# Kernel optimization log

Measured on AMD Instinct MI355X. Metric: run time of the kernel, lower is better.

Reference implementation:

```python
import jax, jax.numpy as jnp
import numpy as np


def _spectral_normalize(W):
    # spectral_norm divides the weight by its largest singular value
    sigma = jnp.linalg.norm(W, ord=2)
    return W / sigma


def setup_inputs() -> dict:
    key = jax.random.key(0)
    ks = jax.random.split(key, 8)
    B, C, H, W = 2, 64, 96, 96
    C8 = C // 8
    x = jax.random.normal(ks[0], (B, C, H, W), dtype=jnp.float32)
    Wq = jax.random.normal(ks[1], (C8, C), dtype=jnp.float32) * 0.1
    bq = jax.random.normal(ks[2], (C8,), dtype=jnp.float32) * 0.1
    Wk = jax.random.normal(ks[3], (C8, C), dtype=jnp.float32) * 0.1
    bk = jax.random.normal(ks[4], (C8,), dtype=jnp.float32) * 0.1
    Wv = jax.random.normal(ks[5], (C, C), dtype=jnp.float32) * 0.1
    bv = jax.random.normal(ks[6], (C,), dtype=jnp.float32) * 0.1
    gamma = jnp.ones((1,), dtype=jnp.float32)
    return {"x": x, "Wq": Wq, "bq": bq, "Wk": Wk, "bk": bk,
            "Wv": Wv, "bv": bv, "gamma": gamma}


def reference(x, Wq, bq, Wk, bk, Wv, bv, gamma):
    B, C, H, W = x.shape
    xf = x.reshape(B, C, H * W)                       # [B, C, N]
    Wq_n = _spectral_normalize(Wq)
    Wk_n = _spectral_normalize(Wk)
    Wv_n = _spectral_normalize(Wv)
    # 1x1 Conv1d == matmul over channel dim
    f = jnp.einsum('oc,bcn->bon', Wq_n, xf) + bq[None, :, None]   # [B, C/8, N]
    g = jnp.einsum('oc,bcn->bon', Wk_n, xf) + bk[None, :, None]   # [B, C/8, N]
    h = jnp.einsum('oc,bcn->bon', Wv_n, xf) + bv[None, :, None]   # [B, C, N]
    # scores[b,i,j] = sum_c f[b,c,i] * g[b,c,j];  softmax over dim=1 (i)
    scores = jnp.einsum('bci,bcj->bij', f, g)                      # [B, N, N]
    beta = jax.nn.softmax(scores, axis=1)
    # o[b,c,j] = sum_i h[b,c,i] * beta[b,i,j]
    o = gamma[0] * jnp.einsum('bci,bij->bcj', h, beta) + xf
    return o.reshape(B, C, H, W)
```

## Files before the change

### kernel.cpp

```cpp
#include <hip/hip_runtime.h>


#define N_PIX 9216
#define N_B   2
#define N_C   64

typedef _Float16 half8  __attribute__((ext_vector_type(8)));
typedef _Float16 half2v __attribute__((ext_vector_type(2)));
typedef float    float4v __attribute__((ext_vector_type(4)));
typedef float    float16v __attribute__((ext_vector_type(16)));
typedef int      int4v  __attribute__((ext_vector_type(4)));

#define LOG2E 1.44269504088896340736f
#define EXP_SHIFT 12.0f

__global__ __launch_bounds__(64) void k_sigma(const float* __restrict__ Wq,
                                              const float* __restrict__ Wk,
                                              const float* __restrict__ Wv,
                                              float* __restrict__ sig,
                                              unsigned* __restrict__ maxKu) {
  __shared__ float G8[8][8];
  __shared__ float Wl[64 * 64];
  __shared__ _Float16 Wh[64 * 80];
  __shared__ _Float16 Gh[64 * 80];
  const int t = threadIdx.x;
  const int mat = blockIdx.x;
  if (mat == 0 && t < 2) maxKu[t] = 0u;
  if (mat < 2) {
    const float* W = (mat == 0) ? Wq : Wk;
    const int i = t >> 3, j = t & 7;
    float g = 0.f;
    for (int c = 0; c < 64; ++c) g += W[i * 64 + c] * W[j * 64 + c];
    G8[i][j] = g;
    __syncthreads();
    const int L = t & 7;
    float G0[8], Gr[8];
    for (int k = 0; k < 8; ++k) { G0[k] = G8[L][k]; Gr[k] = G0[k]; }
    for (int it = 0; it < 8; ++it) {
      float g2[8] = {0, 0, 0, 0, 0, 0, 0, 0};
      for (int k = 0; k < 8; ++k) {
        float gik = Gr[k];
        for (int jj = 0; jj < 8; ++jj) g2[jj] += gik * __shfl(Gr[jj], k, 64);
      }
      float mx = 0.f;
      for (int jj = 0; jj < 8; ++jj) mx = fmaxf(mx, fabsf(g2[jj]));
      for (int d = 1; d < 8; d <<= 1) mx = fmaxf(mx, __shfl_xor(mx, d, 64));
      float r = 1.f / mx;
      for (int jj = 0; jj < 8; ++jj) Gr[jj] = g2[jj] * r;
    }
    float u = 0.f;
    for (int jj = 0; jj < 8; ++jj) u += Gr[jj];
    float y = 0.f;
    for (int k = 0; k < 8; ++k) y += G0[k] * __shfl(u, k, 64);
    float nu = u * y, de = u * u;
    for (int d = 1; d < 8; d <<= 1) { nu += __shfl_xor(nu, d, 64); de += __shfl_xor(de, d, 64); }
    if (t == 0) sig[mat] = sqrtf(nu / de);
  } else {
    for (int idx = t; idx < 4096; idx += 64) Wl[idx] = Wv[idx];
    __syncthreads();
    for (int idx = t; idx < 4096; idx += 64) Wh[(idx >> 6) * 80 + (idx & 63)] = (_Float16)Wl[idx];
    __syncthreads();
    const int lane15 = t & 15, quad = t >> 4;
    half8 fr[4][2];
    for (int rb = 0; rb < 4; ++rb)
      for (int kc = 0; kc < 2; ++kc)
        fr[rb][kc] = *(const half8*)&Wh[(lane15 + 16 * rb) * 80 + 32 * kc + 8 * quad];
    float4v D[4][4];
    for (int mb = 0; mb < 4; ++mb) for (int nb = 0; nb < 4; ++nb) D[mb][nb] = (float4v){0.f, 0.f, 0.f, 0.f};
    for (int kc = 0; kc < 2; ++kc)
      for (int mb = 0; mb < 4; ++mb)
        for (int nb = 0; nb < 4; ++nb)
          D[mb][nb] = __builtin_amdgcn_mfma_f32_16x16x32_f16(fr[mb][kc], fr[nb][kc], D[mb][nb], 0, 0, 0);
    for (int it = 0; it < 8; ++it) {
      float mx = 0.f;
      for (int mb = 0; mb < 4; ++mb) for (int nb = 0; nb < 4; ++nb) for (int r = 0; r < 4; ++r)
        mx = fmaxf(mx, fabsf(D[mb][nb][r]));
      for (int d = 1; d < 64; d <<= 1) mx = fmaxf(mx, __shfl_xor(mx, d, 64));
      float rs = 1.f / mx;
      for (int mb = 0; mb < 4; ++mb) for (int nb = 0; nb < 4; ++nb) for (int r = 0; r < 4; ++r)
        Gh[(4 * quad + r + 16 * mb) * 80 + lane15 + 16 * nb] = (_Float16)(D[mb][nb][r] * rs);
      __syncthreads();
      if (it == 7) break;
      for (int rb = 0; rb < 4; ++rb)
        for (int kc = 0; kc < 2; ++kc)
          fr[rb][kc] = *(const half8*)&Gh[(lane15 + 16 * rb) * 80 + 32 * kc + 8 * quad];
      for (int mb = 0; mb < 4; ++mb) for (int nb = 0; nb < 4; ++nb) D[mb][nb] = (float4v){0.f, 0.f, 0.f, 0.f};
      for (int kc = 0; kc < 2; ++kc)
        for (int mb = 0; mb < 4; ++mb)
          for (int nb = 0; nb < 4; ++nb)
            D[mb][nb] = __builtin_amdgcn_mfma_f32_16x16x32_f16(fr[mb][kc], fr[nb][kc], D[mb][nb], 0, 0, 0);
      __syncthreads();
    }
    float u = 0.f;
    for (int c = 0; c < 64; ++c) u += (float)Gh[t * 80 + c];
    float z = 0.f;
    for (int i2 = 0; i2 < 64; ++i2) z += Wl[i2 * 64 + t] * __shfl(u, i2, 64);
    float nu = z * z, de = u * u;
    for (int d = 1; d < 64; d <<= 1) { nu += __shfl_xor(nu, d, 64); de += __shfl_xor(de, d, 64); }
    if (t == 0) sig[2] = sqrtf(nu / de);
  }
}

__global__ __launch_bounds__(256) void k_fgh(const float* __restrict__ x,
                                             const float* __restrict__ Wq, const float* __restrict__ bq,
                                             const float* __restrict__ Wk, const float* __restrict__ bk,
                                             const float* __restrict__ Wv, const float* __restrict__ bv,
                                             const float* __restrict__ sig,
                                             _Float16* __restrict__ K16,
                                             _Float16* __restrict__ Q16,
                                             _Float16* __restrict__ VT16,
                                             unsigned* __restrict__ maxKu) {
  __shared__ _Float16 Wsh[80 * 64];
  __shared__ float bsh[80];
  const int t = threadIdx.x;
  const float iq = LOG2E / sig[0], ik = 1.0f / sig[1], iv = 1.0f / sig[2];
  for (int idx = t; idx < 80 * 64; idx += 256) {
    const int m = idx >> 6, c = idx & 63;
    float v;
    if (m < 8)       v = Wq[m * 64 + c] * iq;
    else if (m < 16) v = Wk[(m - 8) * 64 + c] * ik;
    else             v = Wv[(m - 16) * 64 + c] * iv;
    Wsh[idx] = (_Float16)v;
  }
  if (t < 80) {
    float v;
    if (t < 8)       v = bq[t] * LOG2E;
    else if (t < 16) v = bk[t - 8];
    else             v = bv[t - 16];
    bsh[t] = v;
  }
  __syncthreads();
  const int wave = t >> 6;
  const int lane = t & 63;
  const int lane15 = lane & 15, quad = lane >> 4;
  const int tile = blockIdx.x * 4 + wave;
  const int b = tile / 576;
  const int n = (tile % 576) * 16 + lane15;
  half8 wf[5][2];
  for (int mb = 0; mb < 5; ++mb)
    for (int kc = 0; kc < 2; ++kc)
      wf[mb][kc] = *(const half8*)&Wsh[(lane15 + 16 * mb) * 64 + 32 * kc + 8 * quad];
  float4v acc[5];
  for (int mb = 0; mb < 5; ++mb) acc[mb] = *(const float4v*)&bsh[16 * mb + 4 * quad];
  const float* xb = x + (size_t)b * N_C * N_PIX;
  for (int kc = 0; kc < 2; ++kc) {
    half8 bf;
    for (int j = 0; j < 8; ++j)
      bf[j] = (_Float16)xb[(size_t)(32 * kc + 8 * quad + j) * N_PIX + n];
    for (int mb = 0; mb < 5; ++mb)
      acc[mb] = __builtin_amdgcn_mfma_f32_16x16x32_f16(wf[mb][kc], bf, acc[mb], 0, 0, 0);
  }
  {
    _Float16* dstK = K16 + ((size_t)b * N_PIX + n) * 8;
    _Float16* dstQ = Q16 + ((size_t)b * N_PIX + n) * 8;
    for (int r = 0; r < 4; ++r) {
      const int m = 4 * quad + r;
      const _Float16 v = (_Float16)acc[0][r];
      if (m < 8) dstK[m] = v; else dstQ[m - 8] = v;
    }
  }
  for (int mb = 1; mb < 5; ++mb)
    for (int r = 0; r < 4; ++r) {
      const int c = 4 * quad + r + 16 * (mb - 1);
      VT16[((size_t)b * N_C + c) * N_PIX + n] = (_Float16)acc[mb][r];
    }
  float sq = 0.f;
  if (quad < 2)
    for (int r = 0; r < 4; ++r) sq += acc[0][r] * acc[0][r];
  sq += __shfl_xor(sq, 16, 64);
  for (int d = 1; d < 64; d <<= 1) sq = fmaxf(sq, __shfl_xor(sq, d, 64));
  if (lane == 0) atomicMax(&maxKu[b], __float_as_uint(sq));
}


__device__ __forceinline__ void gload16(const _Float16* g, _Float16* l) {
  __builtin_amdgcn_global_load_lds(
      (const __attribute__((address_space(1))) void*)g,
      (__attribute__((address_space(3))) void*)l, 16, 0, 0);
}
#define VMWAIT5() asm volatile("s_waitcnt vmcnt(5)" ::: "memory")

__global__ __launch_bounds__(256, 3) void k_attn(const _Float16* __restrict__ K16,
                                                 const _Float16* __restrict__ Q16,
                                                 const _Float16* __restrict__ VT16,
                                                 const unsigned* __restrict__ maxKu,
                                                 const float* __restrict__ x,
                                                 const float* __restrict__ gamma,
                                                 float* __restrict__ out) {
  __shared__ __align__(16) _Float16 SM[4][5120];
  const int wave = threadIdx.x >> 6;
  const int lane = threadIdx.x & 63;
  const int q31 = lane & 31, hi = lane >> 5;
  const int tile = blockIdx.x;
  const int b = tile / 288;
  const int jb = (tile % 288) * 32;
  const float gm = gamma[0];
  const _Float16* Kb = K16 + (size_t)b * N_PIX * 8;
  const _Float16* Vb = VT16 + (size_t)b * N_C * N_PIX;
  _Float16* Rg = SM[wave];
  const int cl = lane >> 2, kk = lane & 3;
  const int gsw = (kk ^ (cl & 3)) * 8;
  const int vq = q31 * 32;
  const int voff00 = vq + (((0 + hi) ^ (q31 & 3)) << 3);
  const int voff01 = vq + (((2 + hi) ^ (q31 & 3)) << 3);
  const int voff10 = 1024 + voff00;
  const int voff11 = 1024 + voff01;

  half8 qf = {};
  if (hi == 0) qf = *(const half8*)(Q16 + ((size_t)b * N_PIX + jb + q31) * 8);
  const float maxK = sqrtf(__uint_as_float(maxKu[b]));
  float nq = 0.f;
#pragma unroll
  for (int j = 0; j < 8; ++j) nq += (float)qf[j] * (float)qf[j];
  nq += __shfl_xor(nq, 32, 64);
  const float M = sqrtf(nq) * maxK - EXP_SHIFT;
  float16v sinit;
#pragma unroll
  for (int r2 = 0; r2 < 16; ++r2) sinit[r2] = -M;

  float16v acc0 = {}, acc1 = {};
  float ls = 0.f;

#define STAGE(SLOT, I0)                                                          \
  {                                                                              \
    const int _i = (I0);                                                         \
    gload16(Kb + (size_t)(_i + q31) * 8, Rg + 4096 + (SLOT) * 512);              \
    gload16(Vb + (size_t)cl * N_PIX + _i + gsw,        Rg + (SLOT) * 2048);      \
    gload16(Vb + (size_t)(16 + cl) * N_PIX + _i + gsw, Rg + (SLOT) * 2048 + 512);\
    gload16(Vb + (size_t)(32 + cl) * N_PIX + _i + gsw, Rg + (SLOT) * 2048 + 1024);\
    gload16(Vb + (size_t)(48 + cl) * N_PIX + _i + gsw, Rg + (SLOT) * 2048 + 1536);\
  }

  STAGE(0, 32 * wave)

#pragma unroll 1
  for (int r = 0; r < 72; ++r) {
    const int slot = r & 1, nslot = slot ^ 1;
    const int i1 = (r < 71) ? (128 * (r + 1) + 32 * wave) : (128 * 71 + 32 * wave);
    STAGE(nslot, i1)
    VMWAIT5();
    half8 kf = *(const half8*)&Rg[4096 + slot * 512 + q31 * 8];
    if (hi) kf = (half8){};
    float16v s = __builtin_amdgcn_mfma_f32_32x32x16_f16(kf, qf, sinit, 0, 0, 0);
    int pk[8];
#pragma unroll
    for (int u = 0; u < 8; ++u) {
      const float p0 = __builtin_amdgcn_exp2f(s[2 * u]);
      const float p1 = __builtin_amdgcn_exp2f(s[2 * u + 1]);
      ls += p0 + p1;
      pk[u] = __builtin_bit_cast(int, __builtin_amdgcn_cvt_pkrtz(p0, p1));
    }
    const int t0 = hi ? pk[0] : pk[2];
    const int t1 = hi ? pk[1] : pk[3];
    const int t2 = hi ? pk[4] : pk[6];
    const int t3 = hi ? pk[5] : pk[7];
    const int x0 = __shfl_xor(t0, 32, 64);
    const int x1 = __shfl_xor(t1, 32, 64);
    const int x2 = __shfl_xor(t2, 32, 64);
    const int x3 = __shfl_xor(t3, 32, 64);
    int4v B0i, B1i;
    B0i[0] = hi ? x0 : pk[0];  B0i[1] = hi ? x1 : pk[1];
    B0i[2] = hi ? pk[2] : x0;  B0i[3] = hi ? pk[3] : x1;
    B1i[0] = hi ? x2 : pk[4];  B1i[1] = hi ? x3 : pk[5];
    B1i[2] = hi ? pk[6] : x2;  B1i[3] = hi ? pk[7] : x3;
    const half8 P0 = __builtin_bit_cast(half8, B0i);
    const half8 P1 = __builtin_bit_cast(half8, B1i);
    const _Float16* Vs = Rg + slot * 2048;
    const half8 v00 = *(const half8*)&Vs[voff00];
    const half8 v01 = *(const half8*)&Vs[voff01];
    const half8 v10 = *(const half8*)&Vs[voff10];
    const half8 v11 = *(const half8*)&Vs[voff11];
    acc0 = __builtin_amdgcn_mfma_f32_32x32x16_f16(v00, P0, acc0, 0, 0, 0);
    acc0 = __builtin_amdgcn_mfma_f32_32x32x16_f16(v01, P1, acc0, 0, 0, 0);
    acc1 = __builtin_amdgcn_mfma_f32_32x32x16_f16(v10, P0, acc1, 0, 0, 0);
    acc1 = __builtin_amdgcn_mfma_f32_32x32x16_f16(v11, P1, acc1, 0, 0, 0);
  }
#undef STAGE
  asm volatile("s_waitcnt vmcnt(0)" ::: "memory");

  float* Ow = (float*)Rg;
  float* Lw = (float*)Rg + 1100;
  ls += __shfl_xor(ls, 32, 64);
  if (hi == 0) Lw[q31] = ls;
#pragma unroll
  for (int r2 = 0; r2 < 16; ++r2) Ow[lane * 17 + r2] = acc0[r2];
  __syncthreads();
  float ltot = 0.f;
#pragma unroll
  for (int w = 0; w < 4; ++w) ltot += ((const float*)SM[w])[1100 + q31];
  const float inv = gm / ltot;
  const float* xb = x + (size_t)b * N_C * N_PIX;
  float* ob = out + (size_t)b * N_C * N_PIX;
#pragma unroll
  for (int r2 = 0; r2 < 16; ++r2) {
    float osum = 0.f;
#pragma unroll
    for (int w = 0; w < 4; ++w) osum += ((const float*)SM[w])[lane * 17 + r2];
    const int c = (r2 & 3) + 8 * (r2 >> 2) + 4 * hi;
    const size_t idx = (size_t)c * N_PIX + jb + q31;
    ob[idx] = osum * inv + xb[idx];
  }
  __syncthreads();
#pragma unroll
  for (int r2 = 0; r2 < 16; ++r2) Ow[lane * 17 + r2] = acc1[r2];
  __syncthreads();
#pragma unroll
  for (int r2 = 0; r2 < 16; ++r2) {
    float osum = 0.f;
#pragma unroll
    for (int w = 0; w < 4; ++w) osum += ((const float*)SM[w])[lane * 17 + r2];
    const int c = 32 + (r2 & 3) + 8 * (r2 >> 2) + 4 * hi;
    const size_t idx = (size_t)c * N_PIX + jb + q31;
    ob[idx] = osum * inv + xb[idx];
  }
}

extern "C" void kernel_launch(void* const* d_in, const int* in_sizes, int n_in,
                              void* d_out, int out_size, void* d_ws, size_t ws_size,
                              hipStream_t stream) {
  const float* x     = (const float*)d_in[0];
  const float* Wq    = (const float*)d_in[1];
  const float* bq    = (const float*)d_in[2];
  const float* Wk    = (const float*)d_in[3];
  const float* bk    = (const float*)d_in[4];
  const float* Wv    = (const float*)d_in[5];
  const float* bv    = (const float*)d_in[6];
  const float* gamma = (const float*)d_in[7];
  float* out = (float*)d_out;

  char* ws = (char*)d_ws;
  float*    sig   = (float*)ws;
  unsigned* maxKu = (unsigned*)(ws + 16);
  _Float16* K16   = (_Float16*)(ws + 10752);
  _Float16* Q16   = (_Float16*)(ws + 10752 + 294912);
  _Float16* VT16  = (_Float16*)(ws + 10752 + 2 * 294912);

  hipLaunchKernelGGL(k_sigma, dim3(3), dim3(64), 0, stream, Wq, Wk, Wv, sig, maxKu);
  hipLaunchKernelGGL(k_fgh, dim3(288), dim3(256), 0, stream,
                     x, Wq, bq, Wk, bk, Wv, bv, sig, K16, Q16, VT16, maxKu);
  hipLaunchKernelGGL(k_attn, dim3(576), dim3(256), 0, stream, K16, Q16, VT16, maxKu, x, gamma, out);
}
```

Baseline: 175.0 us.

## Split attention key range in two and merge partial sums in a new kernel

The attention kernel now splits the key dimension into two halves. This doubles the grid to 1152 blocks, and each block writes unnormalized partial outputs and row sums to workspace. A new merge kernel adds the two partials, normalizes, scales by gamma and adds the residual. Launch bounds are raised to 4 blocks per CU and the LDS swizzle pattern is changed. This raises parallelism for the 256-CU device, since 576 blocks underfill it, at the cost of an extra launch and about 9 MB of partial-sum traffic. Because the shift is a fixed per-row bound, the partials can be summed directly without rescaling.

```diff
diff --git a/kernel.cpp b/kernel.cpp
--- a/kernel.cpp
+++ b/kernel.cpp
@@ -6,7 +6,6 @@
 #define N_C   64
 
 typedef _Float16 half8  __attribute__((ext_vector_type(8)));
-typedef _Float16 half2v __attribute__((ext_vector_type(2)));
 typedef float    float4v __attribute__((ext_vector_type(4)));
 typedef float    float16v __attribute__((ext_vector_type(16)));
 typedef int      int4v  __attribute__((ext_vector_type(4)));
@@ -180,29 +179,30 @@
 }
 #define VMWAIT5() asm volatile("s_waitcnt vmcnt(5)" ::: "memory")
 
-__global__ __launch_bounds__(256, 3) void k_attn(const _Float16* __restrict__ K16,
+__global__ __launch_bounds__(256, 4) void k_attn(const _Float16* __restrict__ K16,
                                                  const _Float16* __restrict__ Q16,
                                                  const _Float16* __restrict__ VT16,
                                                  const unsigned* __restrict__ maxKu,
-                                                 const float* __restrict__ x,
-                                                 const float* __restrict__ gamma,
-                                                 float* __restrict__ out) {
+                                                 float* __restrict__ Opart,
+                                                 float* __restrict__ Lpart) {
   __shared__ __align__(16) _Float16 SM[4][5120];
   const int wave = threadIdx.x >> 6;
   const int lane = threadIdx.x & 63;
   const int q31 = lane & 31, hi = lane >> 5;
   const int tile = blockIdx.x;
-  const int b = tile / 288;
-  const int jb = (tile % 288) * 32;
-  const float gm = gamma[0];
+  const int b = tile / 576;
+  const int rm = tile % 576;
+  const int jb = (rm >> 1) * 32;
+  const int h = rm & 1;
+  const int kh = h * (N_PIX / 2);
   const _Float16* Kb = K16 + (size_t)b * N_PIX * 8;
   const _Float16* Vb = VT16 + (size_t)b * N_C * N_PIX;
   _Float16* Rg = SM[wave];
   const int cl = lane >> 2, kk = lane & 3;
-  const int gsw = (kk ^ (cl & 3)) * 8;
-  const int vq = q31 * 32;
-  const int voff00 = vq + (((0 + hi) ^ (q31 & 3)) << 3);
-  const int voff01 = vq + (((2 + hi) ^ (q31 & 3)) << 3);
+  const int gsw = (kk ^ ((cl >> 1) & 3)) * 8;
+  const int vx = (q31 >> 1) & 3;
+  const int voff00 = q31 * 32 + ((hi ^ vx) << 3);
+  const int voff01 = q31 * 32 + (((2 + hi) ^ vx) << 3);
   const int voff10 = 1024 + voff00;
   const int voff11 = 1024 + voff01;
 
@@ -231,12 +231,12 @@
     gload16(Vb + (size_t)(48 + cl) * N_PIX + _i + gsw, Rg + (SLOT) * 2048 + 1536);\
   }
 
-  STAGE(0, 32 * wave)
+  STAGE(0, kh + 32 * wave)
 
 #pragma unroll 1
-  for (int r = 0; r < 72; ++r) {
+  for (int r = 0; r < 36; ++r) {
     const int slot = r & 1, nslot = slot ^ 1;
-    const int i1 = (r < 71) ? (128 * (r + 1) + 32 * wave) : (128 * 71 + 32 * wave);
+    const int i1 = kh + ((r < 35) ? (128 * (r + 1) + 32 * wave) : (128 * 35 + 32 * wave));
     STAGE(nslot, i1)
     VMWAIT5();
     half8 kf = *(const half8*)&Rg[4096 + slot * 512 + q31 * 8];
@@ -288,30 +288,54 @@
   float ltot = 0.f;
 #pragma unroll
   for (int w = 0; w < 4; ++w) ltot += ((const float*)SM[w])[1100 + q31];
-  const float inv = gm / ltot;
+  float* Op = Opart + (size_t)tile * 2048;
+  if (wave == 0 && hi == 0) Lpart[tile * 32 + q31] = ltot;
+#pragma unroll
+  for (int r2 = 0; r2 < 16; ++r2) {
+    float osum = 0.f;
+#pragma unroll
+    for (int w = 0; w < 4; ++w) osum += ((const float*)SM[w])[lane * 17 + r2];
+    const int c = (r2 & 3) + 8 * (r2 >> 2) + 4 * hi;
+    Op[c * 32 + q31] = osum;
+  }
+  __syncthreads();
+#pragma unroll
+  for (int r2 = 0; r2 < 16; ++r2) Ow[lane * 17 + r2] = acc1[r2];
+  __syncthreads();
+#pragma unroll
+  for (int r2 = 0; r2 < 16; ++r2) {
+    float osum = 0.f;
+#pragma unroll
+    for (int w = 0; w < 4; ++w) osum += ((const float*)SM[w])[lane * 17 + r2];
+    const int c = 32 + (r2 & 3) + 8 * (r2 >> 2) + 4 * hi;
+    Op[c * 32 + q31] = osum;
+  }
+}
+
+__global__ __launch_bounds__(256) void k_merge(const float* __restrict__ Opart,
+                                               const float* __restrict__ Lpart,
+                                               const float* __restrict__ x,
+                                               const float* __restrict__ gamma,
+                                               float* __restrict__ out) {
+  __shared__ float Ls[32];
+  const int t2 = blockIdx.x;
+  const int b = t2 / 288, jt = t2 % 288;
+  const int jb = jt * 32;
+  const int tile0 = b * 576 + jt * 2;
+  const float gm = gamma[0];
+  const int t = threadIdx.x;
+  if (t < 32) Ls[t] = Lpart[tile0 * 32 + t] + Lpart[(tile0 + 1) * 32 + t];
+  __syncthreads();
+  const float* O0 = Opart + (size_t)tile0 * 2048;
+  const float* O1 = O0 + 2048;
   const float* xb = x + (size_t)b * N_C * N_PIX;
   float* ob = out + (size_t)b * N_C * N_PIX;
 #pragma unroll
-  for (int r2 = 0; r2 < 16; ++r2) {
-    float osum = 0.f;
-#pragma unroll
-    for (int w = 0; w < 4; ++w) osum += ((const float*)SM[w])[lane * 17 + r2];
-    const int c = (r2 & 3) + 8 * (r2 >> 2) + 4 * hi;
-    const size_t idx = (size_t)c * N_PIX + jb + q31;
-    ob[idx] = osum * inv + xb[idx];
-  }
-  __syncthreads();
-#pragma unroll
-  for (int r2 = 0; r2 < 16; ++r2) Ow[lane * 17 + r2] = acc1[r2];
-  __syncthreads();
-#pragma unroll
-  for (int r2 = 0; r2 < 16; ++r2) {
-    float osum = 0.f;
-#pragma unroll
-    for (int w = 0; w < 4; ++w) osum += ((const float*)SM[w])[lane * 17 + r2];
-    const int c = 32 + (r2 & 3) + 8 * (r2 >> 2) + 4 * hi;
-    const size_t idx = (size_t)c * N_PIX + jb + q31;
-    ob[idx] = osum * inv + xb[idx];
+  for (int k = 0; k < 8; ++k) {
+    const int idx = t + 256 * k;
+    const int c = idx >> 5, q = idx & 31;
+    const size_t gi = (size_t)c * N_PIX + jb + q;
+    ob[gi] = gm * (O0[idx] + O1[idx]) / Ls[q] + xb[gi];
   }
 }
 
@@ -334,9 +358,12 @@
   _Float16* K16   = (_Float16*)(ws + 10752);
   _Float16* Q16   = (_Float16*)(ws + 10752 + 294912);
   _Float16* VT16  = (_Float16*)(ws + 10752 + 2 * 294912);
+  float*    Opart = (float*)(ws + 2960384);
+  float*    Lpart = (float*)(ws + 2960384 + 9437184);
 
   hipLaunchKernelGGL(k_sigma, dim3(3), dim3(64), 0, stream, Wq, Wk, Wv, sig, maxKu);
   hipLaunchKernelGGL(k_fgh, dim3(288), dim3(256), 0, stream,
                      x, Wq, bq, Wk, bk, Wv, bv, sig, K16, Q16, VT16, maxKu);
-  hipLaunchKernelGGL(k_attn, dim3(576), dim3(256), 0, stream, K16, Q16, VT16, maxKu, x, gamma, out);
-}
+  hipLaunchKernelGGL(k_attn, dim3(1152), dim3(256), 0, stream, K16, Q16, VT16, maxKu, Opart, Lpart);
+  hipLaunchKernelGGL(k_merge, dim3(576), dim3(256), 0, stream, Opart, Lpart, x, gamma, out);
+}
```

Result: no change. 171.9 us (-1.8%).
